# Optimization experiments

Hardware: AMD Instinct MI355X
Metric: run time of the kernel (lower is better)

Reference implementation:

```python
import jax, jax.numpy as jnp
import numpy as np

# DeepSeek-style MLA decode paged attention (vLLM HPU flat_pa_mla, latent cache path)
B = 32              # batch (decode requests)
H = 16              # q heads (TP shard)
KV_LORA = 512       # kv_lora_rank
ROPE = 64           # qk_rope_head_dim
D = KV_LORA + ROPE  # 576, latent+rope dim
BS = 128            # block_size
BLOCKS_PER_SEQ = 16 # 2048-token context
NB = B * BLOCKS_PER_SEQ   # 512 active blocks
NCACHE = 1024       # blocks in the paged cache
SCALE = 192 ** -0.5  # 1/sqrt(qk_nope(128)+rope(64))
NEG = -1.0e9


def setup_inputs() -> dict:
    key = jax.random.key(0)
    k1, k2, k3, k4 = jax.random.split(key, 4)
    query = jax.random.normal(k1, (B, H, D), dtype=jnp.float32)
    key_cache = jax.random.normal(k2, (NCACHE, BS, D), dtype=jnp.float32)
    # each active block points at some cache block
    block_list = jax.random.randint(k3, (NB,), 0, NCACHE, dtype=jnp.int32)
    # contiguous grouping: blocks_per_seq blocks per request
    block_groups = jnp.repeat(jnp.arange(B, dtype=jnp.int32), BLOCKS_PER_SEQ)
    block_mapping = jax.nn.one_hot(block_groups, B, dtype=jnp.float32)  # [NB, B]
    # per-block usage in [1, BS]; unused tail positions masked out
    usage = jax.random.randint(k4, (NB,), 1, BS + 1)
    block_bias = jnp.where(jnp.arange(BS)[None, :] < usage[:, None], 0.0, NEG).astype(jnp.float32)
    return {"query": query, "key_cache": key_cache, "block_mapping": block_mapping,
            "block_bias": block_bias, "block_list": block_list, "block_groups": block_groups}


def reference(query, key_cache, block_mapping, block_bias, block_list, block_groups):
    # batch2block: scatter per-batch query to its blocks via one-hot matmul
    q = SCALE * jnp.einsum('nb,bhd->nhd', block_mapping, query)      # [NB,H,D]
    kv = key_cache[block_list]                                       # [NB,BS,D] fetched latent KV
    v = kv[..., :KV_LORA]                                            # [NB,BS,V]
    attn = jnp.einsum('nhd,nsd->nhs', q, kv) + block_bias[:, None, :]  # [NB,H,BS]
    # per-block online softmax pieces
    block_max = attn.max(axis=-1, keepdims=True)                     # [NB,H,1]
    p = jnp.exp(attn - block_max)
    block_sums = p.sum(axis=-1)                                      # [NB,H]
    o = jnp.einsum('nhs,nsv->nhv', p, v)                             # [NB,H,V]
    bm = block_max[..., 0]                                           # [NB,H]
    # grouped max over blocks of the same request, broadcast back to blocks
    group_max = jax.ops.segment_max(bm, block_groups, num_segments=B)[block_groups]
    adj = jnp.exp(bm - group_max)                                    # [NB,H]
    sum_adj = block_sums * adj
    # block2batch then batch2block of the adjusted sums
    group_sum = jnp.einsum('nb,nh->bh', block_mapping, sum_adj)
    group_sum = jnp.einsum('nb,bh->nh', block_mapping, group_sum)
    group_sum = jnp.maximum(group_sum, sum_adj)
    rescale = adj / group_sum
    o = o * rescale[..., None]
    # block2batch: sum rescaled partial outputs per request
    out = jnp.einsum('nb,nhv->bhv', block_mapping, o)                # [B,H,V]
    return out
```

## Files before the change

kernel.cpp:

```cpp
#include <hip/hip_runtime.h>
#include <math.h>

#define NB_ 512
#define B_ 32
#define H_ 16
#define D_ 576
#define KV_ 512
#define BS_ 128
#define SCALE_ 0.07216878364870323f

__device__ float g_o[NB_ * H_ * KV_];
__device__ float g_bm[NB_ * H_];
__device__ float g_bs[NB_ * H_];

__global__ __launch_bounds__(256) void mla_block_kernel(
    const float* __restrict__ query,
    const float* __restrict__ key_cache,
    const float* __restrict__ block_bias,
    const int* __restrict__ block_list,
    const int* __restrict__ block_groups)
{
    __shared__ float region1[10240];
    __shared__ float kt[128 * 36];
    float* q_s = region1;
    float* vt  = region1;
    float* p_s = region1 + 8192;

    const int tid = threadIdx.x;
    const int n   = blockIdx.x;
    const int b   = block_groups[n];
    const float* K = key_cache + (long)block_list[n] * (BS_ * D_);
    const float* Q = query + (long)b * (H_ * D_);

    {
        const float4* Q4 = (const float4*)Q;
        float4* S4 = (float4*)q_s;
#pragma unroll
        for (int i = 0; i < 9; ++i) {
            int idx = tid + 256 * i;
            float4 v = Q4[idx];
            v.x *= SCALE_; v.y *= SCALE_; v.z *= SCALE_; v.w *= SCALE_;
            S4[idx] = v;
        }
    }

    const int hg = tid >> 6;
    const int sl = tid & 63;

    float acc0[4] = {0.f, 0.f, 0.f, 0.f};
    float acc1[4] = {0.f, 0.f, 0.f, 0.f};

    for (int dc = 0; dc < D_; dc += 32) {
        __syncthreads();
#pragma unroll
        for (int i = 0; i < 4; ++i) {
            int flat = tid + 256 * i;
            int s = flat >> 3;
            int c = (flat & 7) << 2;
            *(float4*)(kt + s * 36 + c) = *(const float4*)(K + (long)s * D_ + dc + c);
        }
        __syncthreads();
#pragma unroll
        for (int d4 = 0; d4 < 32; d4 += 4) {
            float4 k0 = *(const float4*)(kt + sl * 36 + d4);
            float4 k1 = *(const float4*)(kt + (sl + 64) * 36 + d4);
#pragma unroll
            for (int i = 0; i < 4; ++i) {
                float4 qv = *(const float4*)(q_s + (4 * hg + i) * D_ + dc + d4);
                acc0[i] += qv.x * k0.x + qv.y * k0.y + qv.z * k0.z + qv.w * k0.w;
                acc1[i] += qv.x * k1.x + qv.y * k1.y + qv.z * k1.z + qv.w * k1.w;
            }
        }
    }

    float bias0 = block_bias[n * BS_ + sl];
    float bias1 = block_bias[n * BS_ + sl + 64];
    __syncthreads();
#pragma unroll
    for (int i = 0; i < 4; ++i) {
        float a0 = acc0[i] + bias0;
        float a1 = acc1[i] + bias1;
        float m = fmaxf(a0, a1);
#pragma unroll
        for (int off = 32; off; off >>= 1) m = fmaxf(m, __shfl_xor(m, off));
        float p0 = __expf(a0 - m);
        float p1 = __expf(a1 - m);
        float s2 = p0 + p1;
#pragma unroll
        for (int off = 32; off; off >>= 1) s2 += __shfl_xor(s2, off);
        int h = 4 * hg + i;
        p_s[h * BS_ + sl] = p0;
        p_s[h * BS_ + sl + 64] = p1;
        if (sl == 0) {
            g_bm[n * H_ + h] = m;
            g_bs[n * H_ + h] = s2;
        }
    }

    float4 oa0[4], oa1[4];
#pragma unroll
    for (int i = 0; i < 4; ++i) {
        oa0[i] = make_float4(0.f, 0.f, 0.f, 0.f);
        oa1[i] = make_float4(0.f, 0.f, 0.f, 0.f);
    }

    for (int sc = 0; sc < BS_; sc += 16) {
        __syncthreads();
#pragma unroll
        for (int i = 0; i < 8; ++i) {
            int flat = tid + 256 * i;
            int s = flat >> 7;
            int c = (flat & 127) << 2;
            *(float4*)(vt + s * KV_ + c) = *(const float4*)(K + (long)(sc + s) * D_ + c);
        }
        __syncthreads();
#pragma unroll 4
        for (int s = 0; s < 16; ++s) {
            float4 v0 = *(const float4*)(vt + s * KV_ + 4 * sl);
            float4 v1 = *(const float4*)(vt + s * KV_ + 256 + 4 * sl);
#pragma unroll
            for (int i = 0; i < 4; ++i) {
                float pv = p_s[(4 * hg + i) * BS_ + sc + s];
                oa0[i].x += pv * v0.x; oa0[i].y += pv * v0.y;
                oa0[i].z += pv * v0.z; oa0[i].w += pv * v0.w;
                oa1[i].x += pv * v1.x; oa1[i].y += pv * v1.y;
                oa1[i].z += pv * v1.z; oa1[i].w += pv * v1.w;
            }
        }
    }

    float* op = g_o + (long)n * H_ * KV_;
#pragma unroll
    for (int i = 0; i < 4; ++i) {
        *(float4*)(op + (4 * hg + i) * KV_ + 4 * sl) = oa0[i];
        *(float4*)(op + (4 * hg + i) * KV_ + 256 + 4 * sl) = oa1[i];
    }
}

__global__ __launch_bounds__(128) void mla_combine_kernel(float* __restrict__ out)
{
    const int bh = blockIdx.x;
    const int b = bh >> 4;
    const int h = bh & 15;
    const int tid = threadIdx.x;

    float bm[16];
    float m = -1e30f;
#pragma unroll
    for (int j = 0; j < 16; ++j) {
        bm[j] = g_bm[(16 * b + j) * H_ + h];
        m = fmaxf(m, bm[j]);
    }
    float sa[16];
    float gs = 0.f;
#pragma unroll
    for (int j = 0; j < 16; ++j) {
        sa[j] = g_bs[(16 * b + j) * H_ + h] * __expf(bm[j] - m);
        gs += sa[j];
    }
    float4 acc = make_float4(0.f, 0.f, 0.f, 0.f);
#pragma unroll
    for (int j = 0; j < 16; ++j) {
        float r = __expf(bm[j] - m) / fmaxf(gs, sa[j]);
        const float4 v = *(const float4*)(g_o + ((long)((16 * b + j) * H_ + h)) * KV_ + 4 * tid);
        acc.x += r * v.x; acc.y += r * v.y;
        acc.z += r * v.z; acc.w += r * v.w;
    }
    *(float4*)(out + (long)bh * KV_ + 4 * tid) = acc;
}

extern "C" void kernel_launch(void* const* d_in, const int* in_sizes, int n_in,
                              void* d_out, int out_size, void* d_ws, size_t ws_size,
                              hipStream_t stream)
{
    const float* query       = (const float*)d_in[0];
    const float* key_cache   = (const float*)d_in[1];
    const float* block_bias  = (const float*)d_in[3];
    const int*   block_list  = (const int*)d_in[4];
    const int*   block_groups= (const int*)d_in[5];
    float* out = (float*)d_out;

    mla_block_kernel<<<NB_, 256, 0, stream>>>(query, key_cache, block_bias,
                                              block_list, block_groups);
    mla_combine_kernel<<<B_ * H_, 128, 0, stream>>>(out);
}
```

Measured before the change: 398.7 us.

## Fuse QK and PV per 16-row KV chunk with online softmax

Restructures the per-block kernel so each 16-row chunk of the latent KV is loaded once into shared memory and used for both the QK dot products and the PV accumulation. An online softmax with running max and sum rescales the output accumulators per chunk. Before, K was read twice (once in 32-column slices for QK, once for V). This removes the second global read of the V part. The cost is more barriers per chunk, a serial 576-long dot product per thread with only 16 lanes per head, and extra rescaling work.

Result: no change. 403.4 us (+1.2%).

```diff
diff --git a/kernel.cpp b/kernel.cpp
--- a/kernel.cpp
+++ b/kernel.cpp
@@ -7,6 +7,7 @@
 #define D_ 576
 #define KV_ 512
 #define BS_ 128
+#define STR 580
 #define SCALE_ 0.07216878364870323f
 
 __device__ float g_o[NB_ * H_ * KV_];
@@ -20,11 +21,10 @@
     const int* __restrict__ block_list,
     const int* __restrict__ block_groups)
 {
-    __shared__ float region1[10240];
-    __shared__ float kt[128 * 36];
-    float* q_s = region1;
-    float* vt  = region1;
-    float* p_s = region1 + 8192;
+    __shared__ float q_s[H_ * STR];
+    __shared__ float kt[16 * STR];
+    __shared__ float p_s[H_ * 16];
+    __shared__ float alpha_s[H_];
 
     const int tid = threadIdx.x;
     const int n   = blockIdx.x;
@@ -32,71 +32,24 @@
     const float* K = key_cache + (long)block_list[n] * (BS_ * D_);
     const float* Q = query + (long)b * (H_ * D_);
 
-    {
-        const float4* Q4 = (const float4*)Q;
-        float4* S4 = (float4*)q_s;
 #pragma unroll
-        for (int i = 0; i < 9; ++i) {
-            int idx = tid + 256 * i;
-            float4 v = Q4[idx];
-            v.x *= SCALE_; v.y *= SCALE_; v.z *= SCALE_; v.w *= SCALE_;
-            S4[idx] = v;
-        }
+    for (int i = 0; i < 9; ++i) {
+        int flat = tid + 256 * i;
+        int row = flat / 144;
+        int c4  = flat - row * 144;
+        float4 v = *(const float4*)(Q + row * D_ + 4 * c4);
+        v.x *= SCALE_; v.y *= SCALE_; v.z *= SCALE_; v.w *= SCALE_;
+        *(float4*)(q_s + row * STR + 4 * c4) = v;
     }
 
-    const int hg = tid >> 6;
-    const int sl = tid & 63;
+    const int hg  = tid >> 6;
+    const int sl  = tid & 63;
+    const int h2  = sl >> 4;
+    const int s16 = sl & 15;
+    const int h   = 4 * hg + h2;
 
-    float acc0[4] = {0.f, 0.f, 0.f, 0.f};
-    float acc1[4] = {0.f, 0.f, 0.f, 0.f};
-
-    for (int dc = 0; dc < D_; dc += 32) {
-        __syncthreads();
-#pragma unroll
-        for (int i = 0; i < 4; ++i) {
-            int flat = tid + 256 * i;
-            int s = flat >> 3;
-            int c = (flat & 7) << 2;
-            *(float4*)(kt + s * 36 + c) = *(const float4*)(K + (long)s * D_ + dc + c);
-        }
-        __syncthreads();
-#pragma unroll
-        for (int d4 = 0; d4 < 32; d4 += 4) {
-            float4 k0 = *(const float4*)(kt + sl * 36 + d4);
-            float4 k1 = *(const float4*)(kt + (sl + 64) * 36 + d4);
-#pragma unroll
-            for (int i = 0; i < 4; ++i) {
-                float4 qv = *(const float4*)(q_s + (4 * hg + i) * D_ + dc + d4);
-                acc0[i] += qv.x * k0.x + qv.y * k0.y + qv.z * k0.z + qv.w * k0.w;
-                acc1[i] += qv.x * k1.x + qv.y * k1.y + qv.z * k1.z + qv.w * k1.w;
-            }
-        }
-    }
-
-    float bias0 = block_bias[n * BS_ + sl];
-    float bias1 = block_bias[n * BS_ + sl + 64];
-    __syncthreads();
-#pragma unroll
-    for (int i = 0; i < 4; ++i) {
-        float a0 = acc0[i] + bias0;
-        float a1 = acc1[i] + bias1;
-        float m = fmaxf(a0, a1);
-#pragma unroll
-        for (int off = 32; off; off >>= 1) m = fmaxf(m, __shfl_xor(m, off));
-        float p0 = __expf(a0 - m);
-        float p1 = __expf(a1 - m);
-        float s2 = p0 + p1;
-#pragma unroll
-        for (int off = 32; off; off >>= 1) s2 += __shfl_xor(s2, off);
-        int h = 4 * hg + i;
-        p_s[h * BS_ + sl] = p0;
-        p_s[h * BS_ + sl + 64] = p1;
-        if (sl == 0) {
-            g_bm[n * H_ + h] = m;
-            g_bs[n * H_ + h] = s2;
-        }
-    }
-
+    float m_run = -1e30f;
+    float l_run = 0.f;
     float4 oa0[4], oa1[4];
 #pragma unroll
     for (int i = 0; i < 4; ++i) {
@@ -107,20 +60,54 @@
     for (int sc = 0; sc < BS_; sc += 16) {
         __syncthreads();
 #pragma unroll
-        for (int i = 0; i < 8; ++i) {
+        for (int i = 0; i < 9; ++i) {
             int flat = tid + 256 * i;
-            int s = flat >> 7;
-            int c = (flat & 127) << 2;
-            *(float4*)(vt + s * KV_ + c) = *(const float4*)(K + (long)(sc + s) * D_ + c);
+            int row = flat / 144;
+            int c4  = flat - row * 144;
+            *(float4*)(kt + row * STR + 4 * c4) =
+                *(const float4*)(K + (long)(sc + row) * D_ + 4 * c4);
         }
         __syncthreads();
+
+        float acc = 0.f;
+#pragma unroll 4
+        for (int d = 0; d < D_; d += 4) {
+            float4 kv = *(const float4*)(kt + s16 * STR + d);
+            float4 qv = *(const float4*)(q_s + h * STR + d);
+            acc += qv.x * kv.x + qv.y * kv.y + qv.z * kv.z + qv.w * kv.w;
+        }
+        float logit = acc + block_bias[n * BS_ + sc + s16];
+
+        float mc = logit;
+#pragma unroll
+        for (int off = 1; off < 16; off <<= 1) mc = fmaxf(mc, __shfl_xor(mc, off));
+        float m_new = fmaxf(m_run, mc);
+        float alpha = __expf(m_run - m_new);
+        float p = __expf(logit - m_new);
+        float psum = p;
+#pragma unroll
+        for (int off = 1; off < 16; off <<= 1) psum += __shfl_xor(psum, off);
+        l_run = l_run * alpha + psum;
+        m_run = m_new;
+        p_s[h * 16 + s16] = p;
+        if (s16 == 0) alpha_s[h] = alpha;
+        __syncthreads();
+
+        float a[4];
+#pragma unroll
+        for (int i = 0; i < 4; ++i) a[i] = alpha_s[4 * hg + i];
+#pragma unroll
+        for (int i = 0; i < 4; ++i) {
+            oa0[i].x *= a[i]; oa0[i].y *= a[i]; oa0[i].z *= a[i]; oa0[i].w *= a[i];
+            oa1[i].x *= a[i]; oa1[i].y *= a[i]; oa1[i].z *= a[i]; oa1[i].w *= a[i];
+        }
 #pragma unroll 4
         for (int s = 0; s < 16; ++s) {
-            float4 v0 = *(const float4*)(vt + s * KV_ + 4 * sl);
-            float4 v1 = *(const float4*)(vt + s * KV_ + 256 + 4 * sl);
+            float4 v0 = *(const float4*)(kt + s * STR + 4 * sl);
+            float4 v1 = *(const float4*)(kt + s * STR + 256 + 4 * sl);
 #pragma unroll
             for (int i = 0; i < 4; ++i) {
-                float pv = p_s[(4 * hg + i) * BS_ + sc + s];
+                float pv = p_s[(4 * hg + i) * 16 + s];
                 oa0[i].x += pv * v0.x; oa0[i].y += pv * v0.y;
                 oa0[i].z += pv * v0.z; oa0[i].w += pv * v0.w;
                 oa1[i].x += pv * v1.x; oa1[i].y += pv * v1.y;
@@ -129,6 +116,10 @@
         }
     }
 
+    if (s16 == 0) {
+        g_bm[n * H_ + h] = m_run;
+        g_bs[n * H_ + h] = l_run;
+    }
     float* op = g_o + (long)n * H_ * KV_;
 #pragma unroll
     for (int i = 0; i < 4; ++i) {
@@ -173,11 +164,11 @@
                               void* d_out, int out_size, void* d_ws, size_t ws_size,
                               hipStream_t stream)
 {
-    const float* query       = (const float*)d_in[0];
-    const float* key_cache   = (const float*)d_in[1];
-    const float* block_bias  = (const float*)d_in[3];
-    const int*   block_list  = (const int*)d_in[4];
-    const int*   block_groups= (const int*)d_in[5];
+    const float* query        = (const float*)d_in[0];
+    const float* key_cache    = (const float*)d_in[1];
+    const float* block_bias   = (const float*)d_in[3];
+    const int*   block_list   = (const int*)d_in[4];
+    const int*   block_groups = (const int*)d_in[5];
     float* out = (float*)d_out;
 
     mla_block_kernel<<<NB_, 256, 0, stream>>>(query, key_cache, block_bias,
```

## Compute QK^T logits with bf16 MFMA instead of scalar FP32 dot products

Applied to the files above, without the earlier changes.

The Q·K score phase now converts Q and K tiles to bf16 in shared memory and uses the 16x16x32 bf16 MFMA, with each wave covering 32 token rows for all 16 heads. Because each wave only holds part of a head's scores, the softmax max and sum are reduced across waves through small shared arrays. The P·V phase stays in scalar FP32. The aim is to cut the FP32 ALU cost of the 576-dim dot products, at the cost of bf16 rounding error in the logits. A launch-bounds occupancy hint is also added.

Result: no change. 391.9 us (-1.7%).

```diff
diff --git a/kernel.cpp b/kernel.cpp
--- a/kernel.cpp
+++ b/kernel.cpp
@@ -9,22 +9,33 @@
 #define BS_ 128
 #define SCALE_ 0.07216878364870323f
 
+typedef __attribute__((ext_vector_type(8))) short bf16x8;
+typedef __attribute__((ext_vector_type(4))) float f32x4;
+
 __device__ float g_o[NB_ * H_ * KV_];
 __device__ float g_bm[NB_ * H_];
 __device__ float g_bs[NB_ * H_];
 
-__global__ __launch_bounds__(256) void mla_block_kernel(
+static __device__ inline unsigned short f2bf(float f) {
+    unsigned int u = __float_as_uint(f);
+    unsigned int r = (u + 0x7FFFu + ((u >> 16) & 1u)) >> 16;
+    return (unsigned short)r;
+}
+
+__global__ __launch_bounds__(256, 3) void mla_block_kernel(
     const float* __restrict__ query,
     const float* __restrict__ key_cache,
     const float* __restrict__ block_bias,
     const int* __restrict__ block_list,
     const int* __restrict__ block_groups)
 {
-    __shared__ float region1[10240];
-    __shared__ float kt[128 * 36];
-    float* q_s = region1;
-    float* vt  = region1;
-    float* p_s = region1 + 8192;
+    __shared__ unsigned char region[40960];
+    __shared__ float mred[4][16];
+    __shared__ float lred[4][16];
+    unsigned short* qf = (unsigned short*)region;
+    unsigned short* kf = (unsigned short*)(region + 18944);
+    float* vt  = (float*)region;
+    float* p_s = (float*)(region + 32768);
 
     const int tid = threadIdx.x;
     const int n   = blockIdx.x;
@@ -32,86 +43,111 @@
     const float* K = key_cache + (long)block_list[n] * (BS_ * D_);
     const float* Q = query + (long)b * (H_ * D_);
 
-    {
-        const float4* Q4 = (const float4*)Q;
-        float4* S4 = (float4*)q_s;
-#pragma unroll
-        for (int i = 0; i < 9; ++i) {
-            int idx = tid + 256 * i;
-            float4 v = Q4[idx];
-            v.x *= SCALE_; v.y *= SCALE_; v.z *= SCALE_; v.w *= SCALE_;
-            S4[idx] = v;
-        }
-    }
-
-    const int hg = tid >> 6;
-    const int sl = tid & 63;
-
-    float acc0[4] = {0.f, 0.f, 0.f, 0.f};
-    float acc1[4] = {0.f, 0.f, 0.f, 0.f};
-
-    for (int dc = 0; dc < D_; dc += 32) {
-        __syncthreads();
-#pragma unroll
-        for (int i = 0; i < 4; ++i) {
+    const int w    = tid >> 6;
+    const int lane = tid & 63;
+    const int a15  = lane & 15;
+    const int q4   = lane >> 4;
+
+#pragma unroll
+    for (int i = 0; i < 9; ++i) {
+        int flat = tid + 256 * i;
+        int row = flat / 144;
+        int c4  = flat - row * 144;
+        float4 v = *(const float4*)(Q + row * D_ + 4 * c4);
+        ushort4 us;
+        us.x = f2bf(v.x * SCALE_); us.y = f2bf(v.y * SCALE_);
+        us.z = f2bf(v.z * SCALE_); us.w = f2bf(v.w * SCALE_);
+        *(ushort4*)(qf + row * 592 + 4 * c4) = us;
+    }
+
+    f32x4 acc0 = {0.f, 0.f, 0.f, 0.f};
+    f32x4 acc1 = {0.f, 0.f, 0.f, 0.f};
+    for (int kk = 0; kk < 9; ++kk) {
+        __syncthreads();
+#pragma unroll
+        for (int i = 0; i < 8; ++i) {
             int flat = tid + 256 * i;
-            int s = flat >> 3;
-            int c = (flat & 7) << 2;
-            *(float4*)(kt + s * 36 + c) = *(const float4*)(K + (long)s * D_ + dc + c);
-        }
-        __syncthreads();
-#pragma unroll
-        for (int d4 = 0; d4 < 32; d4 += 4) {
-            float4 k0 = *(const float4*)(kt + sl * 36 + d4);
-            float4 k1 = *(const float4*)(kt + (sl + 64) * 36 + d4);
-#pragma unroll
-            for (int i = 0; i < 4; ++i) {
-                float4 qv = *(const float4*)(q_s + (4 * hg + i) * D_ + dc + d4);
-                acc0[i] += qv.x * k0.x + qv.y * k0.y + qv.z * k0.z + qv.w * k0.w;
-                acc1[i] += qv.x * k1.x + qv.y * k1.y + qv.z * k1.z + qv.w * k1.w;
-            }
-        }
-    }
-
-    float bias0 = block_bias[n * BS_ + sl];
-    float bias1 = block_bias[n * BS_ + sl + 64];
+            int s = flat >> 4;
+            int bb = flat & 15;
+            float4 v = *(const float4*)(K + (long)s * D_ + kk * 64 + 4 * bb);
+            ushort4 us;
+            us.x = f2bf(v.x); us.y = f2bf(v.y); us.z = f2bf(v.z); us.w = f2bf(v.w);
+            *(ushort4*)(kf + s * 72 + 4 * bb) = us;
+        }
+        __syncthreads();
+#pragma unroll
+        for (int t = 0; t < 2; ++t) {
+            bf16x8 af  = *(bf16x8*)(qf + a15 * 592 + kk * 64 + t * 32 + 8 * q4);
+            bf16x8 bf0 = *(bf16x8*)(kf + (32 * w + a15) * 72 + t * 32 + 8 * q4);
+            bf16x8 bf1 = *(bf16x8*)(kf + (32 * w + 16 + a15) * 72 + t * 32 + 8 * q4);
+            acc0 = __builtin_amdgcn_mfma_f32_16x16x32_bf16(af, bf0, acc0, 0, 0, 0);
+            acc1 = __builtin_amdgcn_mfma_f32_16x16x32_bf16(af, bf1, acc1, 0, 0, 0);
+        }
+    }
+
+    const float* bias = block_bias + n * BS_;
+    float b0 = bias[32 * w + a15];
+    float b1 = bias[32 * w + 16 + a15];
+    float lg0[4], lg1[4], mw[4];
+#pragma unroll
+    for (int r = 0; r < 4; ++r) {
+        lg0[r] = acc0[r] + b0;
+        lg1[r] = acc1[r] + b1;
+        float m = fmaxf(lg0[r], lg1[r]);
+#pragma unroll
+        for (int off = 1; off < 16; off <<= 1) m = fmaxf(m, __shfl_xor(m, off));
+        mw[r] = m;
+    }
+    if (a15 == 0) {
+#pragma unroll
+        for (int r = 0; r < 4; ++r) mred[w][4 * q4 + r] = mw[r];
+    }
     __syncthreads();
-#pragma unroll
-    for (int i = 0; i < 4; ++i) {
-        float a0 = acc0[i] + bias0;
-        float a1 = acc1[i] + bias1;
-        float m = fmaxf(a0, a1);
-#pragma unroll
-        for (int off = 32; off; off >>= 1) m = fmaxf(m, __shfl_xor(m, off));
-        float p0 = __expf(a0 - m);
-        float p1 = __expf(a1 - m);
-        float s2 = p0 + p1;
-#pragma unroll
-        for (int off = 32; off; off >>= 1) s2 += __shfl_xor(s2, off);
-        int h = 4 * hg + i;
-        p_s[h * BS_ + sl] = p0;
-        p_s[h * BS_ + sl + 64] = p1;
-        if (sl == 0) {
-            g_bm[n * H_ + h] = m;
-            g_bs[n * H_ + h] = s2;
-        }
-    }
-
+    float mg[4], lw[4];
+#pragma unroll
+    for (int r = 0; r < 4; ++r) {
+        int h = 4 * q4 + r;
+        float m = fmaxf(fmaxf(mred[0][h], mred[1][h]), fmaxf(mred[2][h], mred[3][h]));
+        mg[r] = m;
+        float p0 = __expf(lg0[r] - m);
+        float p1 = __expf(lg1[r] - m);
+        p_s[h * BS_ + 32 * w + a15]      = p0;
+        p_s[h * BS_ + 32 * w + 16 + a15] = p1;
+        float s = p0 + p1;
+#pragma unroll
+        for (int off = 1; off < 16; off <<= 1) s += __shfl_xor(s, off);
+        lw[r] = s;
+    }
+    if (a15 == 0) {
+#pragma unroll
+        for (int r = 0; r < 4; ++r) lred[w][4 * q4 + r] = lw[r];
+    }
+    __syncthreads();
+    if (w == 0 && a15 == 0) {
+#pragma unroll
+        for (int r = 0; r < 4; ++r) {
+            int h = 4 * q4 + r;
+            g_bm[n * H_ + h] = mg[r];
+            g_bs[n * H_ + h] = lred[0][h] + lred[1][h] + lred[2][h] + lred[3][h];
+        }
+    }
+
+    const int hg = w;
+    const int sl = lane;
     float4 oa0[4], oa1[4];
 #pragma unroll
     for (int i = 0; i < 4; ++i) {
         oa0[i] = make_float4(0.f, 0.f, 0.f, 0.f);
         oa1[i] = make_float4(0.f, 0.f, 0.f, 0.f);
     }
-
-    for (int sc = 0; sc < BS_; sc += 16) {
+    for (int sc = 0; sc < 8; ++sc) {
         __syncthreads();
 #pragma unroll
         for (int i = 0; i < 8; ++i) {
             int flat = tid + 256 * i;
             int s = flat >> 7;
             int c = (flat & 127) << 2;
-            *(float4*)(vt + s * KV_ + c) = *(const float4*)(K + (long)(sc + s) * D_ + c);
+            *(float4*)(vt + s * KV_ + c) = *(const float4*)(K + (long)(16 * sc + s) * D_ + c);
         }
         __syncthreads();
 #pragma unroll 4
@@ -120,7 +156,7 @@
             float4 v1 = *(const float4*)(vt + s * KV_ + 256 + 4 * sl);
 #pragma unroll
             for (int i = 0; i < 4; ++i) {
-                float pv = p_s[(4 * hg + i) * BS_ + sc + s];
+                float pv = p_s[(4 * hg + i) * BS_ + 16 * sc + s];
                 oa0[i].x += pv * v0.x; oa0[i].y += pv * v0.y;
                 oa0[i].z += pv * v0.z; oa0[i].w += pv * v0.w;
                 oa1[i].x += pv * v1.x; oa1[i].y += pv * v1.y;
@@ -173,11 +209,11 @@
                               void* d_out, int out_size, void* d_ws, size_t ws_size,
                               hipStream_t stream)
 {
-    const float* query       = (const float*)d_in[0];
-    const float* key_cache   = (const float*)d_in[1];
-    const float* block_bias  = (const float*)d_in[3];
-    const int*   block_list  = (const int*)d_in[4];
-    const int*   block_groups= (const int*)d_in[5];
+    const float* query        = (const float*)d_in[0];
+    const float* key_cache    = (const float*)d_in[1];
+    const float* block_bias   = (const float*)d_in[3];
+    const int*   block_list   = (const int*)d_in[4];
+    const int*   block_groups = (const int*)d_in[5];
     float* out = (float*)d_out;
 
     mla_block_kernel<<<NB_, 256, 0, stream>>>(query, key_cache, block_bias,
```
